# Performance work log

Hardware: AMD Instinct MI355X
Metric: run time of the kernel (lower is better)

The kernel has to match this reference:

```python
import jax, jax.numpy as jnp
import numpy as np

N_ORDER = 64
PRED_LEN = 720
SEQ_LEN = 720
ENC_IN = 321
BATCH = 16


def _hippo_legs(N):
    # HiPPO-LegS continuous transition (A, B), float64 numpy
    q = np.arange(N, dtype=np.float64)
    col, row = np.meshgrid(q, q)
    r = 2.0 * q + 1.0
    M = -(np.where(row >= col, r, 0.0) - np.diag(q))
    T = np.sqrt(np.diag(2.0 * q + 1.0))
    A = T @ M @ np.linalg.inv(T)
    B = np.diag(T)[:, None].copy()
    return A, B


def _discretize_bilinear(A, B, dt):
    # scipy.signal.cont2discrete(..., method='bilinear') equivalent
    N = A.shape[0]
    I = np.eye(N)
    BL = np.linalg.inv(I - (dt / 2.0) * A)
    Ad = BL @ (I + (dt / 2.0) * A)
    Bd = (BL @ (dt * B)).squeeze(-1)
    return Ad, Bd


def _legendre_eval_matrix(N, dt):
    # ss.eval_legendre(np.arange(N)[:,None], 1 - 2*vals).T via 3-term recurrence
    vals = np.arange(0.0, 1.0, dt)
    x = 1.0 - 2.0 * vals
    Ps = [np.ones_like(x), x]
    for n in range(1, N - 1):
        Ps.append(((2.0 * n + 1.0) * x * Ps[-1] - n * Ps[-2]) / (n + 1.0))
    return np.stack(Ps[:N], axis=0).T  # [len(vals), N]


def setup_inputs() -> dict:
    key = jax.random.key(0)
    k1, k2, k3 = jax.random.split(key, 3)
    dt = 1.0 / PRED_LEN
    A, B = _hippo_legs(N_ORDER)
    Ad, Bd = _discretize_bilinear(A, B, dt)
    eval_matrix = _legendre_eval_matrix(N_ORDER, dt)
    bound = 1.0 / np.sqrt(N_ORDER)  # torch nn.Linear default init range
    return {
        "x_enc": jax.random.normal(k1, (BATCH, SEQ_LEN, ENC_IN), dtype=jnp.float32),
        "A": jnp.asarray(Ad, dtype=jnp.float32),
        "B_vec": jnp.asarray(Bd, dtype=jnp.float32),
        "eval_matrix": jnp.asarray(eval_matrix, dtype=jnp.float32),
        "W_mlp": jax.random.uniform(k2, (N_ORDER, N_ORDER), jnp.float32, -bound, bound),
        "b_mlp": jax.random.uniform(k3, (N_ORDER,), jnp.float32, -bound, bound),
        "affine_weight": jnp.ones((1, 1, ENC_IN), jnp.float32),
        "affine_bias": jnp.zeros((1, 1, ENC_IN), jnp.float32),
    }


def reference(x_enc, A, B_vec, eval_matrix, W_mlp, b_mlp, affine_weight, affine_bias):
    P, N = eval_matrix.shape  # pred_len, proj_degree

    # RevIN-style instance normalization (means/stdev detached in torch)
    means = jax.lax.stop_gradient(jnp.mean(x_enc, axis=1, keepdims=True))
    x = x_enc - means
    stdev = jax.lax.stop_gradient(jnp.sqrt(jnp.var(x, axis=1, keepdims=True) + 1e-5))
    x = x / stdev
    x = x * affine_weight + affine_bias

    x_in = x[:, -P:]                         # [B, P, E]
    xs = jnp.transpose(x_in, (1, 0, 2))      # [P, B, E]: time-major for scan
    c0 = jnp.zeros((x_in.shape[0], x_in.shape[2], N), x_enc.dtype)

    def step(c, f):
        # c_t = c_{t-1} @ A^T + f_t B  (HiPPO-LegS linear recurrence)
        c_new = c @ A.T + f[..., None] * B_vec
        return c_new, c_new

    _, cs = jax.lax.scan(step, c0, xs)       # [P, B, E, N]

    out1 = cs @ W_mlp.T + b_mlp              # mlp over coefficient dim N
    x_dec_c = out1[P - 1]                    # [B, E, N] (seq_len >= pred_len branch)
    x_dec = x_dec_c @ eval_matrix.T          # [B, E, P] Legendre reconstruction
    x_dec = jnp.transpose(x_dec, (0, 2, 1))  # [B, P, E]

    # de-normalize
    x_dec = (x_dec - affine_bias) / (affine_weight + 1e-10)
    x_dec = x_dec * stdev + means
    return x_dec
```

## Files before the change

kernel.cpp:

```cpp
#include <hip/hip_runtime.h>
#include <math.h>

#define BATCH 16
#define SEQ   720
#define ENC   321
#define NORD  64
#define PRED  720
#define NPAIR (BATCH*ENC)

#define WS_KT    0
#define WS_EWT   (WS_KT + PRED*NORD)
#define WS_EVB   (WS_EWT + NORD*PRED)
#define WS_A16   (WS_EVB + PRED)
#define WS_KSUMP (WS_A16 + 4096)
#define WS_G     (WS_KSUMP + 17*64)
#define WS_PSUM  (WS_G + 4*96*4096)
#define WS_PSS   (WS_PSUM + 4*16*6*64)

#define MV4(AR, SVP, OUTV) do {                                                   \
    float _a0=0.f,_a1=0.f,_a2=0.f,_a3=0.f;                                        \
    _Pragma("unroll")                                                             \
    for (int _k = 0; _k < 4; _k++) {                                              \
        float4 _v0 = *(const float4*)&(SVP)[16*_k];                               \
        float4 _v1 = *(const float4*)&(SVP)[16*_k+4];                             \
        float4 _v2 = *(const float4*)&(SVP)[16*_k+8];                             \
        float4 _v3 = *(const float4*)&(SVP)[16*_k+12];                            \
        _a0 += (AR)[16*_k+0]*_v0.x + (AR)[16*_k+1]*_v0.y                          \
             + (AR)[16*_k+2]*_v0.z + (AR)[16*_k+3]*_v0.w;                         \
        _a1 += (AR)[16*_k+4]*_v1.x + (AR)[16*_k+5]*_v1.y                          \
             + (AR)[16*_k+6]*_v1.z + (AR)[16*_k+7]*_v1.w;                         \
        _a2 += (AR)[16*_k+8]*_v2.x + (AR)[16*_k+9]*_v2.y                          \
             + (AR)[16*_k+10]*_v2.z + (AR)[16*_k+11]*_v2.w;                       \
        _a3 += (AR)[16*_k+12]*_v3.x + (AR)[16*_k+13]*_v3.y                        \
             + (AR)[16*_k+14]*_v3.z + (AR)[16*_k+15]*_v3.w;                       \
    }                                                                             \
    OUTV = (_a0+_a1)+(_a2+_a3);                                                   \
} while (0)

__global__ __launch_bounds__(256, 1) void prep(const float* __restrict__ A,
        const float* __restrict__ Bv, float* __restrict__ ws)
{
    __shared__ float sv[4][64];
    const int tid  = threadIdx.x;
    const int lane = tid & 63;
    const int wv   = tid >> 6;
    if (blockIdx.x < 16) {
        float ar[64];
        #pragma unroll
        for (int k = 0; k < 16; k++) {
            float4 v = *(const float4*)&A[lane*64 + 4*k];
            ar[4*k]=v.x; ar[4*k+1]=v.y; ar[4*k+2]=v.z; ar[4*k+3]=v.w;
        }
        const int j = blockIdx.x*4 + wv;
        sv[wv][lane] = (lane == j) ? 1.f : 0.f;
        for (int s = 0; s < 16; s++) {
            float nv;
            MV4(ar, &sv[wv][0], nv);
            sv[wv][lane] = nv;
        }
        ws[WS_A16 + lane*64 + j] = sv[wv][lane];
    } else {
        if (tid >= 64) return;
        float ar[64];
        #pragma unroll
        for (int k = 0; k < 16; k++) {
            float4 v = *(const float4*)&A[lane*64 + 4*k];
            ar[4*k]=v.x; ar[4*k+1]=v.y; ar[4*k+2]=v.z; ar[4*k+3]=v.w;
        }
        float* Kt = ws + WS_KT;
        float bv = Bv[lane];
        sv[0][lane] = bv;
        Kt[(size_t)719*64 + lane] = bv;
        float ksml = bv;
        for (int j = 1; j <= 15; j++) {
            float nv;
            MV4(ar, &sv[0][0], nv);
            sv[0][lane] = nv;
            Kt[(size_t)(719 - j)*64 + lane] = nv;
            ksml += nv;
        }
        ws[WS_KSUMP + 16*64 + lane] = ksml;
    }
}

__global__ __launch_bounds__(256, 1) void chainsEW(const float* __restrict__ evalm,
        const float* __restrict__ W, const float* __restrict__ bm,
        float* __restrict__ ws)
{
    __shared__ float dsm[64*61];
    const int tid  = threadIdx.x;
    const int lane = tid & 63;
    const int wv   = tid >> 6;
    if (blockIdx.x < 16) {
        if (tid >= 64) return;
        float* sv = dsm;
        const int r = blockIdx.x;
        const float* A16 = ws + WS_A16;
        float* Kt = ws + WS_KT;
        float ar16[64];
        #pragma unroll
        for (int k = 0; k < 16; k++) {
            float4 v = *(const float4*)&A16[lane*64 + 4*k];
            ar16[4*k]=v.x; ar16[4*k+1]=v.y; ar16[4*k+2]=v.z; ar16[4*k+3]=v.w;
        }
        float ksml = 0.f;
        sv[lane] = Kt[(size_t)(719 - r)*64 + lane];
        for (int j = r + 16; j <= 719; j += 16) {
            float nv;
            MV4(ar16, sv, nv);
            sv[lane] = nv;
            Kt[(size_t)(719 - j)*64 + lane] = nv;
            ksml += nv;
        }
        ws[WS_KSUMP + r*64 + lane] = ksml;
    } else {
        float* Et = dsm;
        const int r = blockIdx.x - 16;
        float wcol[64];
        #pragma unroll
        for (int n = 0; n < 64; n++) wcol[n] = W[n*64 + lane];
        float bv = bm[lane];
        #pragma unroll
        for (int k = 0; k < 15; k++) {
            int row = wv + k*4;
            int tp = r*60 + row;
            const float* ev = evalm + (size_t)tp*64;
            float a0=0.f,a1=0.f,a2=0.f,a3=0.f;
            #pragma unroll
            for (int kk = 0; kk < 4; kk++) {
                float4 e0_ = *(const float4*)&ev[16*kk];
                float4 e1_ = *(const float4*)&ev[16*kk+4];
                float4 e2_ = *(const float4*)&ev[16*kk+8];
                float4 e3_ = *(const float4*)&ev[16*kk+12];
                a0 += e0_.x*wcol[16*kk+0] + e0_.y*wcol[16*kk+1]
                    + e0_.z*wcol[16*kk+2] + e0_.w*wcol[16*kk+3];
                a1 += e1_.x*wcol[16*kk+4] + e1_.y*wcol[16*kk+5]
                    + e1_.z*wcol[16*kk+6] + e1_.w*wcol[16*kk+7];
                a2 += e2_.x*wcol[16*kk+8] + e2_.y*wcol[16*kk+9]
                    + e2_.z*wcol[16*kk+10] + e2_.w*wcol[16*kk+11];
                a3 += e3_.x*wcol[16*kk+12] + e3_.y*wcol[16*kk+13]
                    + e3_.z*wcol[16*kk+14] + e3_.w*wcol[16*kk+15];
            }
            Et[lane*61 + row] = (a0+a1)+(a2+a3);
            float pv = ev[lane] * bv;
            #pragma unroll
            for (int o = 32; o > 0; o >>= 1) pv += __shfl_down(pv, o);
            if (lane == 0) ws[WS_EVB + tp] = pv;
        }
        __syncthreads();
        for (int idx = tid; idx < 4096; idx += 256) {
            int m = idx >> 6, row = idx & 63;
            if (row < 60)
                ws[WS_EWT + (size_t)m*720 + r*60 + row] = Et[m*61 + row];
        }
    }
}

__device__ inline float4 ldx(const float* __restrict__ x, int b, int t, int e4)
{
    float4 r = make_float4(0.f,0.f,0.f,0.f);
    const float* p = x + ((size_t)b*SEQ + t)*ENC;
    if (e4 + 3 < ENC) r = *(const float4*)&p[e4];
    else {
        if (e4   < ENC) r.x = p[e4];
        if (e4+1 < ENC) r.y = p[e4+1];
        if (e4+2 < ENC) r.z = p[e4+2];
    }
    return r;
}

__global__ __launch_bounds__(256) void k2(const float* __restrict__ x,
        float* __restrict__ ws)
{
    __shared__ float xt[2][12*64];
    __shared__ float redn[12*64];
    __shared__ float reds[12*64];
    const int tid = threadIdx.x;
    const int bid = blockIdx.x;
    const int b = bid / 24, rem = bid % 24;
    const int et = rem / 4, tsp = rem % 4;
    const int e0 = et*64, t0 = tsp*180;

    const bool xon = tid < 192;
    const int sx_t  = tid >> 4;
    const int sx_e4 = (tid & 15) * 4;

    const float* Kt = ws + WS_KT;
    float s0=0,s1=0,s2=0,s3=0, q0=0,q1=0,q2=0,q3=0;
    float4 rx = make_float4(0,0,0,0);

    if (xon) {
        rx = ldx(x, b, t0 + sx_t, e0 + sx_e4);
        *(float4*)&xt[0][sx_t*64 + sx_e4] = rx;
        s0+=rx.x; s1+=rx.y; s2+=rx.z; s3+=rx.w;
        q0+=rx.x*rx.x; q1+=rx.y*rx.y; q2+=rx.z*rx.z; q3+=rx.w*rx.w;
    }

    const int elg = tid & 15;
    const int mgr = tid >> 4;
    float acc[4][4];
    #pragma unroll
    for (int j = 0; j < 4; j++)
        #pragma unroll
        for (int i = 0; i < 4; i++) acc[j][i] = 0.f;

    for (int ch = 0; ch < 15; ch++) {
        if (ch + 1 < 15 && xon)
            rx = ldx(x, b, t0 + (ch+1)*12 + sx_t, e0 + sx_e4);
        __syncthreads();
        const float* xb = xt[ch & 1];
        const float* kp = Kt + (size_t)(t0 + ch*12)*64 + mgr*4;
        #pragma unroll
        for (int tt = 0; tt < 12; tt++) {
            float4 fa = *(const float4*)&xb[tt*64 + elg*4];
            float4 kv = *(const float4*)&kp[tt*64];
            acc[0][0]+=fa.x*kv.x; acc[0][1]+=fa.x*kv.y; acc[0][2]+=fa.x*kv.z; acc[0][3]+=fa.x*kv.w;
            acc[1][0]+=fa.y*kv.x; acc[1][1]+=fa.y*kv.y; acc[1][2]+=fa.y*kv.z; acc[1][3]+=fa.y*kv.w;
            acc[2][0]+=fa.z*kv.x; acc[2][1]+=fa.z*kv.y; acc[2][2]+=fa.z*kv.z; acc[2][3]+=fa.z*kv.w;
            acc[3][0]+=fa.w*kv.x; acc[3][1]+=fa.w*kv.y; acc[3][2]+=fa.w*kv.z; acc[3][3]+=fa.w*kv.w;
        }
        if (ch + 1 < 15 && xon) {
            *(float4*)&xt[(ch+1)&1][sx_t*64 + sx_e4] = rx;
            s0+=rx.x; s1+=rx.y; s2+=rx.z; s3+=rx.w;
            q0+=rx.x*rx.x; q1+=rx.y*rx.y; q2+=rx.z*rx.z; q3+=rx.w*rx.w;
        }
    }

    float* g = ws + WS_G + (size_t)(tsp*96 + b*6 + et)*4096;
    #pragma unroll
    for (int i = 0; i < 4; i++)
        *(float4*)&g[(mgr*4 + i)*64 + elg*4] =
            make_float4(acc[0][i], acc[1][i], acc[2][i], acc[3][i]);

    __syncthreads();
    if (xon) {
        redn[sx_t*64 + sx_e4+0] = s0; redn[sx_t*64 + sx_e4+1] = s1;
        redn[sx_t*64 + sx_e4+2] = s2; redn[sx_t*64 + sx_e4+3] = s3;
        reds[sx_t*64 + sx_e4+0] = q0; reds[sx_t*64 + sx_e4+1] = q1;
        reds[sx_t*64 + sx_e4+2] = q2; reds[sx_t*64 + sx_e4+3] = q3;
    }
    __syncthreads();
    if (tid < 64) {
        float s = 0.f, q = 0.f;
        #pragma unroll
        for (int rr = 0; rr < 12; rr++) { s += redn[rr*64 + tid]; q += reds[rr*64 + tid]; }
        const size_t o = (size_t)((tsp*16 + b)*6 + et)*64 + tid;
        ws[WS_PSUM + o] = s;
        ws[WS_PSS  + o] = q;
    }
}

#define K3ROW(r, wvv) \
    acc[r][0]+=(wvv)*c0.x; acc[r][1]+=(wvv)*c0.y; acc[r][2]+=(wvv)*c0.z; acc[r][3]+=(wvv)*c0.w; \
    acc[r][4]+=(wvv)*c1.x; acc[r][5]+=(wvv)*c1.y; acc[r][6]+=(wvv)*c1.z; acc[r][7]+=(wvv)*c1.w;

__global__ __launch_bounds__(256) void k3f(const float* __restrict__ aw,
        const float* __restrict__ ab, const float* __restrict__ ws,
        float* __restrict__ out)
{
    __shared__ float Cm[64*192];
    __shared__ float EWm[64*196];
    __shared__ float ssc[128], ssh[128], sP[128], sQ[128];
    __shared__ float kss[64];
    const int tid = threadIdx.x;
    const int b   = blockIdx.x / 12;
    const int rr  = blockIdx.x % 12;
    const int eT  = rr >> 2;
    const int tq  = rr & 3;
    const int e0  = eT * 128;
    const int et0 = eT * 2;

    if (tid < 128) {
        const int el = tid, e = e0 + el;
        const int et = et0 + (el >> 6), eli = el & 63;
        float s = 0.f, q = 0.f;
        #pragma unroll
        for (int tsp = 0; tsp < 4; tsp++) {
            const size_t o = (size_t)((tsp*16 + b)*6 + et)*64 + eli;
            s += ws[WS_PSUM + o];
            q += ws[WS_PSS  + o];
        }
        float mean = s * (1.0f/SEQ);
        float var  = q * (1.0f/SEQ) - mean*mean;
        float sd   = sqrtf(var + 1e-5f);
        if (e < ENC) {
            float a = aw[e], av = ab[e];
            float sc = a / sd;
            float P  = sd / (a + 1e-10f);
            ssc[el] = sc; ssh[el] = av - mean*sc;
            sP[el]  = P;  sQ[el]  = mean - av*P;
        } else {
            ssc[el]=0.f; ssh[el]=0.f; sP[el]=0.f; sQ[el]=0.f;
        }
    }
    if (tid < 64) {
        float s = 0.f;
        #pragma unroll
        for (int p = 0; p < 17; p++) s += ws[WS_KSUMP + p*64 + tid];
        kss[tid] = s;
    }
    __syncthreads();

    const float* G = ws + WS_G;
    #pragma unroll
    for (int k = 0; k < 8; k++) {
        int slot = k*256 + tid;
        int m = slot >> 5, el4 = (slot & 31) * 4;
        int et = et0 + (el4 >> 6), eli4 = el4 & 63;
        size_t base = (size_t)(b*6 + et)*4096 + m*64 + eli4;
        float4 g0 = *(const float4*)&G[base];
        float4 g1 = *(const float4*)&G[base + (size_t) 96*4096];
        float4 g2 = *(const float4*)&G[base + (size_t)192*4096];
        float4 g3 = *(const float4*)&G[base + (size_t)288*4096];
        float km = kss[m];
        float4 sc = *(const float4*)&ssc[el4];
        float4 sh = *(const float4*)&ssh[el4];
        float4 c;
        c.x = sc.x*(g0.x+g1.x+g2.x+g3.x) + sh.x*km;
        c.y = sc.y*(g0.y+g1.y+g2.y+g3.y) + sh.y*km;
        c.z = sc.z*(g0.z+g1.z+g2.z+g3.z) + sh.z*km;
        c.w = sc.w*(g0.w+g1.w+g2.w+g3.w) + sh.w*km;
        *(float4*)&Cm[m*192 + (el4>>3)*12 + (el4&7)] = c;
    }

    const float* EWT = ws + WS_EWT;
    #pragma unroll
    for (int it = 0; it < 12; it++) {
        int slot = it*256 + tid;
        int m = slot / 48, t4 = (slot % 48) * 4;
        int tp = tq*192 + t4;
        float4 v;
        if (tp + 3 < PRED) v = *(const float4*)&EWT[(size_t)m*720 + tp];
        else {
            v = make_float4(0.f,0.f,0.f,0.f);
            if (tp   < PRED) v.x = EWT[(size_t)m*720 + tp];
            if (tp+1 < PRED) v.y = EWT[(size_t)m*720 + tp+1];
            if (tp+2 < PRED) v.z = EWT[(size_t)m*720 + tp+2];
        }
        *(float4*)&EWm[m*196 + t4] = v;
    }
    __syncthreads();

    const int tx = tid & 15;
    const int ty = tid >> 4;
    float acc[12][8];
    #pragma unroll
    for (int r = 0; r < 12; r++)
        #pragma unroll
        for (int j = 0; j < 8; j++) acc[r][j] = 0.f;

    const float* cb = Cm  + tx*12;
    const float* wb = EWm + ty*12;
    #pragma unroll 2
    for (int m = 0; m < 64; m++) {
        float4 c0 = *(const float4*)&cb[m*192];
        float4 c1 = *(const float4*)&cb[m*192 + 4];
        float4 w0 = *(const float4*)&wb[m*196];
        float4 w1 = *(const float4*)&wb[m*196 + 4];
        float4 w2 = *(const float4*)&wb[m*196 + 8];
        K3ROW(0,  w0.x) K3ROW(1,  w0.y) K3ROW(2,  w0.z) K3ROW(3,  w0.w)
        K3ROW(4,  w1.x) K3ROW(5,  w1.y) K3ROW(6,  w1.z) K3ROW(7,  w1.w)
        K3ROW(8,  w2.x) K3ROW(9,  w2.y) K3ROW(10, w2.z) K3ROW(11, w2.w)
    }

    const int elb = tx*8;
    const int eb  = e0 + elb;
    float4 Pa = *(const float4*)&sP[elb];
    float4 Pb = *(const float4*)&sP[elb+4];
    float4 Qa = *(const float4*)&sQ[elb];
    float4 Qb = *(const float4*)&sQ[elb+4];
    const float* evb = ws + WS_EVB;
    #pragma unroll
    for (int r = 0; r < 12; r++) {
        int tp = tq*192 + ty*12 + r;
        if (tp < PRED) {
            float ev = evb[tp];
            float* op = out + ((size_t)b*PRED + tp)*ENC;
            if (eb + 7 < ENC) {
                float4 o0, o1;
                o0.x = (acc[r][0]+ev)*Pa.x + Qa.x;
                o0.y = (acc[r][1]+ev)*Pa.y + Qa.y;
                o0.z = (acc[r][2]+ev)*Pa.z + Qa.z;
                o0.w = (acc[r][3]+ev)*Pa.w + Qa.w;
                o1.x = (acc[r][4]+ev)*Pb.x + Qb.x;
                o1.y = (acc[r][5]+ev)*Pb.y + Qb.y;
                o1.z = (acc[r][6]+ev)*Pb.z + Qb.z;
                o1.w = (acc[r][7]+ev)*Pb.w + Qb.w;
                *(float4*)&op[eb]   = o0;
                *(float4*)&op[eb+4] = o1;
            } else {
                if (eb   < ENC) op[eb  ] = (acc[r][0]+ev)*Pa.x + Qa.x;
                if (eb+1 < ENC) op[eb+1] = (acc[r][1]+ev)*Pa.y + Qa.y;
                if (eb+2 < ENC) op[eb+2] = (acc[r][2]+ev)*Pa.z + Qa.z;
                if (eb+3 < ENC) op[eb+3] = (acc[r][3]+ev)*Pa.w + Qa.w;
                if (eb+4 < ENC) op[eb+4] = (acc[r][4]+ev)*Pb.x + Qb.x;
                if (eb+5 < ENC) op[eb+5] = (acc[r][5]+ev)*Pb.y + Qb.y;
                if (eb+6 < ENC) op[eb+6] = (acc[r][6]+ev)*Pb.z + Qb.z;
                if (eb+7 < ENC) op[eb+7] = (acc[r][7]+ev)*Pb.w + Qb.w;
            }
        }
    }
}

extern "C" void kernel_launch(void* const* d_in, const int* in_sizes, int n_in,
                              void* d_out, int out_size, void* d_ws, size_t ws_size,
                              hipStream_t stream)
{
    const float* x     = (const float*)d_in[0];
    const float* A     = (const float*)d_in[1];
    const float* Bv    = (const float*)d_in[2];
    const float* evalm = (const float*)d_in[3];
    const float* W     = (const float*)d_in[4];
    const float* bm    = (const float*)d_in[5];
    const float* aw    = (const float*)d_in[6];
    const float* ab    = (const float*)d_in[7];
    float* ws  = (float*)d_ws;
    float* out = (float*)d_out;

    prep    <<<17, 256, 0, stream>>>(A, Bv, ws);
    chainsEW<<<28, 256, 0, stream>>>(evalm, W, bm, ws);
    k2      <<<BATCH*6*4, 256, 0, stream>>>(x, ws);
    k3f     <<<192, 256, 0, stream>>>(aw, ab, ws, out);
}
```

Measured before the change: 144.1 us.

## Compute impulse-response chain with A^32 stride and fold EW prep into first kernel

The kernel powers of A that build the response table are now split into 32 interleaved chains using A^32 instead of 16 chains using A^16. This roughly halves the serial matvec depth of the chain kernel. A^32 is computed with 64 single-wave blocks of 32 steps each, and the head chain now runs 31 steps. The eval/W projection work moves into the prep kernel so it overlaps with the A^32 computation. In exchange, the prep stage has a longer serial chain (32 steps versus 16), and raising a matrix to a higher power may change rounding slightly.

```diff
diff --git a/kernel.cpp b/kernel.cpp
--- a/kernel.cpp
+++ b/kernel.cpp
@@ -6,14 +6,13 @@
 #define ENC   321
 #define NORD  64
 #define PRED  720
-#define NPAIR (BATCH*ENC)
 
 #define WS_KT    0
 #define WS_EWT   (WS_KT + PRED*NORD)
 #define WS_EVB   (WS_EWT + NORD*PRED)
-#define WS_A16   (WS_EVB + PRED)
-#define WS_KSUMP (WS_A16 + 4096)
-#define WS_G     (WS_KSUMP + 17*64)
+#define WS_A32   (WS_EVB + PRED)
+#define WS_KSUMP (WS_A32 + 4096)
+#define WS_G     (WS_KSUMP + 33*64)
 #define WS_PSUM  (WS_G + 4*96*4096)
 #define WS_PSS   (WS_PSUM + 4*16*6*64)
 
@@ -37,53 +36,16 @@
     OUTV = (_a0+_a1)+(_a2+_a3);                                                   \
 } while (0)
 
+#define LOADROW(AR, SRC) do {                                                     \
+    _Pragma("unroll")                                                             \
+    for (int _k = 0; _k < 16; _k++) {                                             \
+        float4 _v = *(const float4*)&(SRC)[lane*64 + 4*_k];                       \
+        (AR)[4*_k]=_v.x; (AR)[4*_k+1]=_v.y; (AR)[4*_k+2]=_v.z; (AR)[4*_k+3]=_v.w; \
+    }                                                                             \
+} while (0)
+
 __global__ __launch_bounds__(256, 1) void prep(const float* __restrict__ A,
-        const float* __restrict__ Bv, float* __restrict__ ws)
-{
-    __shared__ float sv[4][64];
-    const int tid  = threadIdx.x;
-    const int lane = tid & 63;
-    const int wv   = tid >> 6;
-    if (blockIdx.x < 16) {
-        float ar[64];
-        #pragma unroll
-        for (int k = 0; k < 16; k++) {
-            float4 v = *(const float4*)&A[lane*64 + 4*k];
-            ar[4*k]=v.x; ar[4*k+1]=v.y; ar[4*k+2]=v.z; ar[4*k+3]=v.w;
-        }
-        const int j = blockIdx.x*4 + wv;
-        sv[wv][lane] = (lane == j) ? 1.f : 0.f;
-        for (int s = 0; s < 16; s++) {
-            float nv;
-            MV4(ar, &sv[wv][0], nv);
-            sv[wv][lane] = nv;
-        }
-        ws[WS_A16 + lane*64 + j] = sv[wv][lane];
-    } else {
-        if (tid >= 64) return;
-        float ar[64];
-        #pragma unroll
-        for (int k = 0; k < 16; k++) {
-            float4 v = *(const float4*)&A[lane*64 + 4*k];
-            ar[4*k]=v.x; ar[4*k+1]=v.y; ar[4*k+2]=v.z; ar[4*k+3]=v.w;
-        }
-        float* Kt = ws + WS_KT;
-        float bv = Bv[lane];
-        sv[0][lane] = bv;
-        Kt[(size_t)719*64 + lane] = bv;
-        float ksml = bv;
-        for (int j = 1; j <= 15; j++) {
-            float nv;
-            MV4(ar, &sv[0][0], nv);
-            sv[0][lane] = nv;
-            Kt[(size_t)(719 - j)*64 + lane] = nv;
-            ksml += nv;
-        }
-        ws[WS_KSUMP + 16*64 + lane] = ksml;
-    }
-}
-
-__global__ __launch_bounds__(256, 1) void chainsEW(const float* __restrict__ evalm,
+        const float* __restrict__ Bv, const float* __restrict__ evalm,
         const float* __restrict__ W, const float* __restrict__ bm,
         float* __restrict__ ws)
 {
@@ -91,31 +53,41 @@
     const int tid  = threadIdx.x;
     const int lane = tid & 63;
     const int wv   = tid >> 6;
-    if (blockIdx.x < 16) {
+    const int bid  = blockIdx.x;
+    if (bid < 64) {
         if (tid >= 64) return;
+        float ar[64];
+        LOADROW(ar, A);
+        const int j = bid;
         float* sv = dsm;
-        const int r = blockIdx.x;
-        const float* A16 = ws + WS_A16;
+        sv[lane] = (lane == j) ? 1.f : 0.f;
+        for (int s = 0; s < 32; s++) {
+            float nv;
+            MV4(ar, sv, nv);
+            sv[lane] = nv;
+        }
+        ws[WS_A32 + lane*64 + j] = sv[lane];
+    } else if (bid == 64) {
+        if (tid >= 64) return;
+        float ar[64];
+        LOADROW(ar, A);
         float* Kt = ws + WS_KT;
-        float ar16[64];
-        #pragma unroll
-        for (int k = 0; k < 16; k++) {
-            float4 v = *(const float4*)&A16[lane*64 + 4*k];
-            ar16[4*k]=v.x; ar16[4*k+1]=v.y; ar16[4*k+2]=v.z; ar16[4*k+3]=v.w;
-        }
-        float ksml = 0.f;
-        sv[lane] = Kt[(size_t)(719 - r)*64 + lane];
-        for (int j = r + 16; j <= 719; j += 16) {
+        float bv = Bv[lane];
+        float* sv = dsm;
+        sv[lane] = bv;
+        Kt[(size_t)719*64 + lane] = bv;
+        float ksml = bv;
+        for (int j = 1; j <= 31; j++) {
             float nv;
-            MV4(ar16, sv, nv);
+            MV4(ar, sv, nv);
             sv[lane] = nv;
             Kt[(size_t)(719 - j)*64 + lane] = nv;
             ksml += nv;
         }
-        ws[WS_KSUMP + r*64 + lane] = ksml;
+        ws[WS_KSUMP + 32*64 + lane] = ksml;
     } else {
         float* Et = dsm;
-        const int r = blockIdx.x - 16;
+        const int r = bid - 65;
         float wcol[64];
         #pragma unroll
         for (int n = 0; n < 64; n++) wcol[n] = W[n*64 + lane];
@@ -156,6 +128,30 @@
     }
 }
 
+__global__ __launch_bounds__(256, 1) void chains32(float* __restrict__ ws)
+{
+    __shared__ float dsm[64];
+    const int tid  = threadIdx.x;
+    const int lane = tid & 63;
+    if (tid >= 64) return;
+    const int r = blockIdx.x;
+    const float* A32 = ws + WS_A32;
+    float* Kt = ws + WS_KT;
+    float ar[64];
+    LOADROW(ar, A32);
+    float* sv = dsm;
+    sv[lane] = Kt[(size_t)(719 - r)*64 + lane];
+    float ksml = 0.f;
+    for (int j = r + 32; j <= 719; j += 32) {
+        float nv;
+        MV4(ar, sv, nv);
+        sv[lane] = nv;
+        Kt[(size_t)(719 - j)*64 + lane] = nv;
+        ksml += nv;
+    }
+    ws[WS_KSUMP + r*64 + lane] = ksml;
+}
+
 __device__ inline float4 ldx(const float* __restrict__ x, int b, int t, int e4)
 {
     float4 r = make_float4(0.f,0.f,0.f,0.f);
@@ -295,8 +291,7 @@
     }
     if (tid < 64) {
         float s = 0.f;
-        #pragma unroll
-        for (int p = 0; p < 17; p++) s += ws[WS_KSUMP + p*64 + tid];
+        for (int p = 0; p < 33; p++) s += ws[WS_KSUMP + p*64 + tid];
         kss[tid] = s;
     }
     __syncthreads();
@@ -417,8 +412,8 @@
     float* ws  = (float*)d_ws;
     float* out = (float*)d_out;
 
-    prep    <<<17, 256, 0, stream>>>(A, Bv, ws);
-    chainsEW<<<28, 256, 0, stream>>>(evalm, W, bm, ws);
+    prep    <<<77, 256, 0, stream>>>(A, Bv, evalm, W, bm, ws);
+    chains32<<<32, 256, 0, stream>>>(ws);
     k2      <<<BATCH*6*4, 256, 0, stream>>>(x, ws);
     k3f     <<<192, 256, 0, stream>>>(aw, ab, ws, out);
 }
```

After: 147.0 us. +2.0%, slower.
